# Performance work log

Measured on AMD Instinct MI355X. Metric: run time of the kernel, lower is better.

The kernel has to match this reference:

```python
import jax, jax.numpy as jnp
import numpy as np

B, SQ, SK, D = 8, 512, 512, 32


def _spd_cov(key, b, s, d):
    # random SPD covariance: A A^T + I
    a = 0.1 * jax.random.normal(key, (b, s, d, d), dtype=jnp.float32)
    return jnp.einsum('bsde,bsfe->bsdf', a, a) + jnp.eye(d, dtype=jnp.float32)


def setup_inputs() -> dict:
    key = jax.random.key(0)
    ks = jax.random.split(key, 6)
    return {
        'q_mean': jax.random.normal(ks[0], (B, SQ, D), dtype=jnp.float32),
        'q_cov': _spd_cov(ks[1], B, SQ, D),
        'k_mean': jax.random.normal(ks[2], (B, SK, D), dtype=jnp.float32),
        'k_cov': _spd_cov(ks[3], B, SK, D),
        'v_mean': jax.random.normal(ks[4], (B, SK, D), dtype=jnp.float32),
        'v_cov': _spd_cov(ks[5], B, SK, D),
    }


def reference(q_mean, q_cov, k_mean, k_cov, v_mean, v_cov):
    # Pairwise symmetric Gaussian JSD attention.
    # JSD = 0.5*(KL(p_q||p_k)+KL(p_k||p_q)); the log-det terms cancel:
    # JSD = 0.25*( tr(Sk^-1 Sq) + tr(Sq^-1 Sk) - 2D
    #              + dm^T (Sk^-1 + Sq^-1) dm ),  dm = mu_q - mu_k
    d = q_mean.shape[-1]
    q_inv = jnp.linalg.inv(q_cov)            # [B,Sq,D,D]
    k_inv = jnp.linalg.inv(k_cov)            # [B,Sk,D,D]
    tr_kq = jnp.einsum('bkde,bqed->bqk', k_inv, q_cov)
    tr_qk = jnp.einsum('bqde,bked->bqk', q_inv, k_cov)
    dm = q_mean[:, :, None, :] - k_mean[:, None, :, :]   # [B,Sq,Sk,D]
    quad = (jnp.einsum('bqkd,bkde,bqke->bqk', dm, k_inv, dm)
            + jnp.einsum('bqkd,bqde,bqke->bqk', dm, q_inv, dm))
    js = 0.25 * (tr_kq + tr_qk - 2.0 * d + quad)         # [B,Sq,Sk]
    score = jax.nn.softmax(js, axis=-1)
    out_mean = jnp.einsum('bqk,bkd->bqd', score, v_mean)
    out_cov = jnp.einsum('bqk,bkde->bqde', score, v_cov)
    return out_mean, out_cov
```

## Files before the change

### kernel.cpp

```cpp
#include <hip/hip_runtime.h>

#define NBATCH 8
#define SQL 512
#define SKL 512
#define DD 32
#define KF 1152
#define UT 528
#define NOUT 1056
#define NVT 1088

typedef short short8 __attribute__((ext_vector_type(8)));
typedef float f32x4 __attribute__((ext_vector_type(4)));
typedef unsigned short ushort_t;

__device__ __forceinline__ ushort_t f2bf(float f) {
    unsigned int u = __float_as_uint(f);
    return (ushort_t)((u + 0x7fffu + ((u >> 16) & 1u)) >> 16);
}
__device__ __forceinline__ float bf2f(ushort_t h) {
    return __uint_as_float(((unsigned int)h) << 16);
}
__device__ __forceinline__ void wsplit(ushort_t* __restrict__ h, ushort_t* __restrict__ l,
                                       size_t idx, float v) {
    ushort_t hb = f2bf(v);
    h[idx] = hb;
    l[idx] = f2bf(v - bf2f(hb));
}
__device__ __forceinline__ float rdlane(float x, int l) {
    return __int_as_float(__builtin_amdgcn_readlane(__float_as_int(x), l));
}
__device__ __forceinline__ void gl_lds16(const ushort_t* g, ushort_t* l) {
    __builtin_amdgcn_global_load_lds(
        (const __attribute__((address_space(1))) void*)g,
        (__attribute__((address_space(3))) void*)l, 16, 0, 0);
}

__global__ __launch_bounds__(256, 8) void feat_kernel(
    const float* __restrict__ qm, const float* __restrict__ qc,
    const float* __restrict__ km, const float* __restrict__ kc,
    ushort_t* __restrict__ fqh, ushort_t* __restrict__ fql,
    ushort_t* __restrict__ fkh, ushort_t* __restrict__ fkl)
{
    const int wid = threadIdx.x >> 6;
    const int lane = threadIdx.x & 63;
    const int gsite = blockIdx.x * 4 + wid;
    const int qside = gsite < NBATCH * SQL;
    const int site = qside ? gsite : gsite - NBATCH * SQL;

    const float* mean = qside ? qm : km;
    const float* cov  = qside ? qc : kc;
    ushort_t* fh = qside ? fqh : fkh;
    ushort_t* fl = qside ? fql : fkl;

    const float* covp = cov + (size_t)site * (DD * DD);
    const float* mup  = mean + (size_t)site * DD;
    const size_t fo = (size_t)site * KF;

    __shared__ float inv_s4[4][DD][DD + 1];
    __shared__ float mu_s4[4][DD];
    __shared__ float iv_s4[4][DD];
    float (*inv_s)[DD + 1] = inv_s4[wid];
    float* mu_s = mu_s4[wid];
    float* iv_s = iv_s4[wid];

    if (lane < DD) mu_s[lane] = mup[lane];

    float a[DD];
    if (lane < DD) {
        #pragma unroll
        for (int r = 0; r < DD; ++r) a[r] = covp[r * DD + lane];
    } else {
        const int c = lane - DD;
        #pragma unroll
        for (int r = 0; r < DD; ++r) a[r] = (r == c) ? 1.0f : 0.0f;
    }

    #pragma unroll
    for (int p = 0; p < DD; ++p) {
        float piv = rdlane(a[p], p);
        float rinv = 1.0f / piv;
        float t = a[p] * rinv;
        #pragma unroll
        for (int r = 0; r < DD; ++r) {
            if (r != p) {
                float fr = rdlane(a[r], p);
                a[r] = fmaf(-fr, t, a[r]);
            }
        }
        a[p] = t;
    }

    if (lane >= DD) {
        const int c = lane - DD;
        #pragma unroll
        for (int r = 0; r < DD; ++r) inv_s[r][c] = a[r];
    }
    __syncthreads();

    if (lane < DD) {
        float s = 0.f;
        #pragma unroll
        for (int e = 0; e < DD; ++e) s += inv_s[lane][e] * mu_s[e];
        iv_s[lane] = s;
    }
    __syncthreads();

    float bias = 0.f;
    #pragma unroll
    for (int d2 = 0; d2 < DD; ++d2) bias += mu_s[d2] * iv_s[d2];

    for (int idx = lane; idx < UT; idx += 64) {
        int d = (int)((65.0f - sqrtf(4225.0f - 8.0f * (float)idx)) * 0.5f);
        if (d > 0 && (d * (65 - d)) / 2 > idx) --d;
        if (((d + 1) * (64 - d)) / 2 <= idx) ++d;
        int off = (d * (65 - d)) / 2;
        int e = d + (idx - off);
        float Mv = covp[d * DD + e] + mu_s[d] * mu_s[e];
        float Iv = 0.5f * (inv_s[d][e] + inv_s[e][d]);
        float w = (d == e) ? 0.25f : 0.5f;
        if (qside) { wsplit(fh, fl, fo + idx, w * Mv); wsplit(fh, fl, fo + UT + idx, w * Iv); }
        else       { wsplit(fh, fl, fo + idx, Iv);     wsplit(fh, fl, fo + UT + idx, Mv); }
    }
    if (lane < DD) {
        float ivv = iv_s[lane], muv = mu_s[lane];
        if (qside) { wsplit(fh, fl, fo + 2*UT + lane, -0.5f * ivv); wsplit(fh, fl, fo + 2*UT + DD + lane, 0.25f * muv); }
        else       { wsplit(fh, fl, fo + 2*UT + lane, muv);         wsplit(fh, fl, fo + 2*UT + DD + lane, -2.f * ivv); }
    }
    if (lane == 32) wsplit(fh, fl, fo + 2*UT + 2*DD, qside ? 0.25f : bias);
    for (int i = 2*UT + 2*DD + 1 + lane; i < KF; i += 64) { fh[fo + i] = 0; fl[fo + i] = 0; }
}

template<int KSTRIDE, int KITERS, int MODE>
__global__ __launch_bounds__(256) void gemm_split(
    const ushort_t* __restrict__ Ah_g, const ushort_t* __restrict__ Al_g,
    const ushort_t* __restrict__ Bh_g, const ushort_t* __restrict__ Bl_g,
    float* __restrict__ C0, float* __restrict__ C1)
{
    constexpr bool ASPLIT = (MODE == 0);
    const int b = blockIdx.z, mt = blockIdx.y, nt = blockIdx.x;
    const int tid = threadIdx.x, lane = tid & 63, wid = tid >> 6;
    const int wm = wid & 1, wn = wid >> 1;
    const int BROWS = MODE ? NVT : SKL;

    const ushort_t* Ah = Ah_g + ((size_t)b * SQL + mt * 128) * KSTRIDE;
    const ushort_t* Al = Al_g + ((size_t)b * SQL + mt * 128) * KSTRIDE;
    const ushort_t* Bh = Bh_g + ((size_t)b * BROWS + nt * 64) * KSTRIDE;
    const ushort_t* Bl = Bl_g + ((size_t)b * BROWS + nt * 64) * KSTRIDE;

    __shared__ __align__(16) ushort_t AsH[128 * 32];
    __shared__ __align__(16) ushort_t AsL[ASPLIT ? 128 * 32 : 8];
    __shared__ __align__(16) ushort_t BsH[64 * 32];
    __shared__ __align__(16) ushort_t BsL[64 * 32];

    const int r4 = lane >> 2, kp = (lane & 3) * 8;
    const int arow0 = wid * 16 + r4,        aoff0 = wid * 512 + lane * 8;
    const int arow1 = (wid + 4) * 16 + r4,  aoff1 = (wid + 4) * 512 + lane * 8;

    const int fm = lane & 15;
    const int q8 = (lane >> 4) * 8;

    f32x4 acc[4][2];
    #pragma unroll
    for (int i = 0; i < 4; ++i)
        #pragma unroll
        for (int j = 0; j < 2; ++j)
            acc[i][j] = (f32x4){0.f, 0.f, 0.f, 0.f};

    for (int it = 0; it < KITERS; ++it) {
        const int k0 = it * 32;
        __syncthreads();
        gl_lds16(Ah + (size_t)arow0 * KSTRIDE + k0 + kp, &AsH[aoff0]);
        gl_lds16(Ah + (size_t)arow1 * KSTRIDE + k0 + kp, &AsH[aoff1]);
        if (ASPLIT) {
            gl_lds16(Al + (size_t)arow0 * KSTRIDE + k0 + kp, &AsL[aoff0]);
            gl_lds16(Al + (size_t)arow1 * KSTRIDE + k0 + kp, &AsL[aoff1]);
        }
        gl_lds16(Bh + (size_t)arow0 * KSTRIDE + k0 + kp, &BsH[aoff0]);
        gl_lds16(Bl + (size_t)arow0 * KSTRIDE + k0 + kp, &BsL[aoff0]);
        __syncthreads();

        short8 ah[4], al[4], bh[2], bl[2];
        #pragma unroll
        for (int i = 0; i < 4; ++i) {
            const int r = wm * 64 + i * 16 + fm;
            ah[i] = *(const short8*)&AsH[r * 32 + q8];
            if (ASPLIT) al[i] = *(const short8*)&AsL[r * 32 + q8];
        }
        #pragma unroll
        for (int j = 0; j < 2; ++j) {
            const int r = wn * 32 + j * 16 + fm;
            bh[j] = *(const short8*)&BsH[r * 32 + q8];
            bl[j] = *(const short8*)&BsL[r * 32 + q8];
        }
        #pragma unroll
        for (int i = 0; i < 4; ++i)
            #pragma unroll
            for (int j = 0; j < 2; ++j) {
                acc[i][j] = __builtin_amdgcn_mfma_f32_16x16x32_bf16(ah[i], bh[j], acc[i][j], 0, 0, 0);
                acc[i][j] = __builtin_amdgcn_mfma_f32_16x16x32_bf16(ah[i], bl[j], acc[i][j], 0, 0, 0);
                if (ASPLIT)
                    acc[i][j] = __builtin_amdgcn_mfma_f32_16x16x32_bf16(al[i], bh[j], acc[i][j], 0, 0, 0);
            }
    }

    const int crow0 = (lane >> 4) * 4;
    const int ccol = lane & 15;
    #pragma unroll
    for (int i = 0; i < 4; ++i) {
        const int m = mt * 128 + wm * 64 + i * 16 + crow0;
        #pragma unroll
        for (int j = 0; j < 2; ++j) {
            const int n = nt * 64 + wn * 32 + j * 16 + ccol;
            #pragma unroll
            for (int r = 0; r < 4; ++r) {
                const float v = acc[i][j][r];
                const size_t rowb = (size_t)b * SQL + (m + r);
                if (MODE == 0) {
                    C0[rowb * SKL + n] = v;
                } else {
                    if (n < DD)        C0[rowb * DD + n] = v;
                    else if (n < NOUT) C1[rowb * (DD * DD) + (n - DD)] = v;
                }
            }
        }
    }
}

__global__ __launch_bounds__(256) void softmax_rows(
    const float* __restrict__ js, ushort_t* __restrict__ ph)
{
    const float* p = js + (size_t)blockIdx.x * SKL;
    const int tid = threadIdx.x;
    float2 v = *(const float2*)(p + 2 * tid);
    float m = fmaxf(v.x, v.y);
    #pragma unroll
    for (int o = 32; o > 0; o >>= 1) m = fmaxf(m, __shfl_xor(m, o));
    __shared__ float redm[4], reds[4];
    const int wid = tid >> 6, ln = tid & 63;
    if (ln == 0) redm[wid] = m;
    __syncthreads();
    m = fmaxf(fmaxf(redm[0], redm[1]), fmaxf(redm[2], redm[3]));
    float e0 = __expf(v.x - m), e1 = __expf(v.y - m);
    float s = e0 + e1;
    #pragma unroll
    for (int o = 32; o > 0; o >>= 1) s += __shfl_xor(s, o);
    if (ln == 0) reds[wid] = s;
    __syncthreads();
    s = reds[0] + reds[1] + reds[2] + reds[3];
    float rs = 1.0f / s;
    size_t o = (size_t)blockIdx.x * SKL + 2 * tid;
    ph[o]     = f2bf(e0 * rs);
    ph[o + 1] = f2bf(e1 * rs);
}

__global__ __launch_bounds__(256) void vsplit_kernel(
    const float* __restrict__ vmean, const float* __restrict__ vcov,
    ushort_t* __restrict__ vth, ushort_t* __restrict__ vtl)
{
    __shared__ float t[32][33];
    const int n0 = blockIdx.x * 32, k0 = blockIdx.y * 32, b = blockIdx.z;
    const int tx = threadIdx.x, ty = threadIdx.y;
    for (int r = ty; r < 32; r += 8) {
        const int k = k0 + r, n = n0 + tx;
        float v;
        if (n0 == 0)          v = vmean[((size_t)b * SKL + k) * DD + n];
        else if (n0 >= NOUT)  v = 0.f;
        else                  v = vcov[((size_t)b * SKL + k) * (DD * DD) + (n - DD)];
        t[tx][r] = v;
    }
    __syncthreads();
    for (int r = ty; r < 32; r += 8) {
        const int n = n0 + r, k = k0 + tx;
        const float v = t[r][tx];
        wsplit(vth, vtl, ((size_t)b * NVT + n) * SKL + k, v);
    }
}

extern "C" void kernel_launch(void* const* d_in, const int* in_sizes, int n_in,
                              void* d_out, int out_size, void* d_ws, size_t ws_size,
                              hipStream_t stream)
{
    const float* q_mean = (const float*)d_in[0];
    const float* q_cov  = (const float*)d_in[1];
    const float* k_mean = (const float*)d_in[2];
    const float* k_cov  = (const float*)d_in[3];
    const float* v_mean = (const float*)d_in[4];
    const float* v_cov  = (const float*)d_in[5];

    float* out_mean = (float*)d_out;
    float* out_cov  = out_mean + (size_t)NBATCH * SQL * DD;

    char* w = (char*)d_ws;
    const size_t FQN = (size_t)NBATCH * SQL * KF;
    ushort_t* fq_h = (ushort_t*)w;
    ushort_t* fq_l = fq_h + FQN;
    ushort_t* fk_h = fq_l + FQN;
    ushort_t* fk_l = fk_h + FQN;
    float*    js   = (float*)(fk_l + FQN);
    ushort_t* vt_h = fq_h;
    ushort_t* vt_l = fq_l;
    ushort_t* p_h  = fk_h;

    feat_kernel<<<dim3(2 * NBATCH * SQL / 4), 256, 0, stream>>>(
        q_mean, q_cov, k_mean, k_cov, fq_h, fq_l, fk_h, fk_l);
    gemm_split<KF, KF / 32, 0><<<dim3(SKL / 64, SQL / 128, NBATCH), 256, 0, stream>>>(
        fq_h, fq_l, fk_h, fk_l, js, nullptr);
    vsplit_kernel<<<dim3(NVT / 32, SKL / 32, NBATCH), dim3(32, 8), 0, stream>>>(
        v_mean, v_cov, vt_h, vt_l);
    softmax_rows<<<NBATCH * SQL, 256, 0, stream>>>(js, p_h);
    gemm_split<SKL, SKL / 32, 1><<<dim3(NVT / 64, SQL / 128, NBATCH), 256, 0, stream>>>(
        p_h, nullptr, vt_h, vt_l, out_mean, out_cov);
}
```

Measured before the change: 225.1 us.

## Split-K score GEMM, drop bf16 low part for V GEMM, fuse softmax and V transpose

The score GEMM now splits K into two halves across more blocks and accumulates into a zeroed buffer with atomicAdd, which raises parallelism at the cost of a memset and atomics. The output GEMM drops the low-order bf16 correction for V and uses a single MFMA per tile, removing one MFMA and one LDS stream but lowering output precision. Softmax and the V transpose are merged into one launch to save a launch. The feature kernel stores the inverse in a packed upper-triangular layout and converts values in pairs to bf16.

```diff
diff --git a/kernel.cpp b/kernel.cpp
--- a/kernel.cpp
+++ b/kernel.cpp
@@ -1,4 +1,5 @@
 #include <hip/hip_runtime.h>
+#include <hip/hip_bf16.h>
 
 #define NBATCH 8
 #define SQL 512
@@ -8,6 +9,9 @@
 #define UT 528
 #define NOUT 1056
 #define NVT 1088
+#define NSITE (NBATCH * SQL)
+#define FEAT_BLOCKS (2 * NSITE / 4)
+#define VS_BLOCKS (34 * 16 * NBATCH)
 
 typedef short short8 __attribute__((ext_vector_type(8)));
 typedef float f32x4 __attribute__((ext_vector_type(4)));
@@ -19,12 +23,6 @@
 }
 __device__ __forceinline__ float bf2f(ushort_t h) {
     return __uint_as_float(((unsigned int)h) << 16);
-}
-__device__ __forceinline__ void wsplit(ushort_t* __restrict__ h, ushort_t* __restrict__ l,
-                                       size_t idx, float v) {
-    ushort_t hb = f2bf(v);
-    h[idx] = hb;
-    l[idx] = f2bf(v - bf2f(hb));
 }
 __device__ __forceinline__ float rdlane(float x, int l) {
     return __int_as_float(__builtin_amdgcn_readlane(__float_as_int(x), l));
@@ -33,6 +31,15 @@
     __builtin_amdgcn_global_load_lds(
         (const __attribute__((address_space(1))) void*)g,
         (__attribute__((address_space(3))) void*)l, 16, 0, 0);
+}
+__device__ __forceinline__ void pk_split(float v0, float v1, ushort_t& h0, ushort_t& h1,
+                                         ushort_t& l0, ushort_t& l1) {
+    __hip_bfloat162 H = __float22bfloat162_rn(make_float2(v0, v1));
+    ushort2 hu = *(ushort2*)&H;
+    h0 = hu.x; h1 = hu.y;
+    __hip_bfloat162 L = __float22bfloat162_rn(make_float2(v0 - bf2f(hu.x), v1 - bf2f(hu.y)));
+    ushort2 lu = *(ushort2*)&L;
+    l0 = lu.x; l1 = lu.y;
 }
 
 __global__ __launch_bounds__(256, 8) void feat_kernel(
@@ -41,11 +48,12 @@
     ushort_t* __restrict__ fqh, ushort_t* __restrict__ fql,
     ushort_t* __restrict__ fkh, ushort_t* __restrict__ fkl)
 {
+    __shared__ float smem[4 * 624];
     const int wid = threadIdx.x >> 6;
     const int lane = threadIdx.x & 63;
     const int gsite = blockIdx.x * 4 + wid;
-    const int qside = gsite < NBATCH * SQL;
-    const int site = qside ? gsite : gsite - NBATCH * SQL;
+    const int qside = gsite < NSITE;
+    const int site = qside ? gsite : gsite - NSITE;
 
     const float* mean = qside ? qm : km;
     const float* cov  = qside ? qc : kc;
@@ -56,12 +64,9 @@
     const float* mup  = mean + (size_t)site * DD;
     const size_t fo = (size_t)site * KF;
 
-    __shared__ float inv_s4[4][DD][DD + 1];
-    __shared__ float mu_s4[4][DD];
-    __shared__ float iv_s4[4][DD];
-    float (*inv_s)[DD + 1] = inv_s4[wid];
-    float* mu_s = mu_s4[wid];
-    float* iv_s = iv_s4[wid];
+    float* inv_p = smem + wid * 624;
+    float* mu_s  = inv_p + 560;
+    float* iv_s  = mu_s + 32;
 
     if (lane < DD) mu_s[lane] = mup[lane];
 
@@ -93,15 +98,22 @@
     if (lane >= DD) {
         const int c = lane - DD;
         #pragma unroll
-        for (int r = 0; r < DD; ++r) inv_s[r][c] = a[r];
+        for (int r = 0; r < DD; ++r)
+            if (r <= c) inv_p[((r * (65 - r)) >> 1) + (c - r)] = a[r];
     }
     __syncthreads();
 
-    if (lane < DD) {
+    {
+        const int j = lane & 31;
+        const int basej = (j * (65 - j)) >> 1;
         float s = 0.f;
         #pragma unroll
-        for (int e = 0; e < DD; ++e) s += inv_s[lane][e] * mu_s[e];
-        iv_s[lane] = s;
+        for (int e = 0; e < DD; ++e) {
+            const int be = (e * (65 - e)) >> 1;
+            const int addr = (e < j) ? (be + (j - e)) : (basej + (e - j));
+            s += inv_p[addr] * mu_s[e];
+        }
+        if (lane < DD) iv_s[lane] = s;
     }
     __syncthreads();
 
@@ -116,28 +128,47 @@
         int off = (d * (65 - d)) / 2;
         int e = d + (idx - off);
         float Mv = covp[d * DD + e] + mu_s[d] * mu_s[e];
-        float Iv = 0.5f * (inv_s[d][e] + inv_s[e][d]);
+        float Iv = inv_p[idx];
         float w = (d == e) ? 0.25f : 0.5f;
-        if (qside) { wsplit(fh, fl, fo + idx, w * Mv); wsplit(fh, fl, fo + UT + idx, w * Iv); }
-        else       { wsplit(fh, fl, fo + idx, Iv);     wsplit(fh, fl, fo + UT + idx, Mv); }
+        float v0, v1;
+        if (qside) { v0 = w * Mv; v1 = w * Iv; }
+        else       { v0 = Iv;     v1 = Mv; }
+        ushort_t h0, h1, l0, l1;
+        pk_split(v0, v1, h0, h1, l0, l1);
+        fh[fo + idx] = h0; fh[fo + UT + idx] = h1;
+        fl[fo + idx] = l0; fl[fo + UT + idx] = l1;
     }
     if (lane < DD) {
         float ivv = iv_s[lane], muv = mu_s[lane];
-        if (qside) { wsplit(fh, fl, fo + 2*UT + lane, -0.5f * ivv); wsplit(fh, fl, fo + 2*UT + DD + lane, 0.25f * muv); }
-        else       { wsplit(fh, fl, fo + 2*UT + lane, muv);         wsplit(fh, fl, fo + 2*UT + DD + lane, -2.f * ivv); }
-    }
-    if (lane == 32) wsplit(fh, fl, fo + 2*UT + 2*DD, qside ? 0.25f : bias);
+        float v0, v1;
+        if (qside) { v0 = -0.5f * ivv; v1 = 0.25f * muv; }
+        else       { v0 = muv;         v1 = -2.f * ivv; }
+        ushort_t h0, h1, l0, l1;
+        pk_split(v0, v1, h0, h1, l0, l1);
+        fh[fo + 2*UT + lane] = h0; fh[fo + 2*UT + DD + lane] = h1;
+        fl[fo + 2*UT + lane] = l0; fl[fo + 2*UT + DD + lane] = l1;
+    }
+    if (lane == 32) {
+        float v = qside ? 0.25f : bias;
+        ushort_t hb = f2bf(v);
+        fh[fo + 2*UT + 2*DD] = hb;
+        fl[fo + 2*UT + 2*DD] = f2bf(v - bf2f(hb));
+    }
     for (int i = 2*UT + 2*DD + 1 + lane; i < KF; i += 64) { fh[fo + i] = 0; fl[fo + i] = 0; }
 }
 
-template<int KSTRIDE, int KITERS, int MODE>
+template<int MODE>
 __global__ __launch_bounds__(256) void gemm_split(
     const ushort_t* __restrict__ Ah_g, const ushort_t* __restrict__ Al_g,
     const ushort_t* __restrict__ Bh_g, const ushort_t* __restrict__ Bl_g,
     float* __restrict__ C0, float* __restrict__ C1)
 {
-    constexpr bool ASPLIT = (MODE == 0);
-    const int b = blockIdx.z, mt = blockIdx.y, nt = blockIdx.x;
+    constexpr bool SPLIT = (MODE == 0);
+    constexpr int KSTRIDE = SPLIT ? KF : SKL;
+    constexpr int KITERS = SPLIT ? (KF / 2 / 32) : (SKL / 32);
+    const int b = blockIdx.z, nt = blockIdx.x;
+    const int mt = SPLIT ? (blockIdx.y & 3) : blockIdx.y;
+    const int kbase = SPLIT ? ((blockIdx.y >> 2) * (KF / 2)) : 0;
     const int tid = threadIdx.x, lane = tid & 63, wid = tid >> 6;
     const int wm = wid & 1, wn = wid >> 1;
     const int BROWS = MODE ? NVT : SKL;
@@ -148,9 +179,9 @@
     const ushort_t* Bl = Bl_g + ((size_t)b * BROWS + nt * 64) * KSTRIDE;
 
     __shared__ __align__(16) ushort_t AsH[128 * 32];
-    __shared__ __align__(16) ushort_t AsL[ASPLIT ? 128 * 32 : 8];
+    __shared__ __align__(16) ushort_t AsL[SPLIT ? 128 * 32 : 8];
     __shared__ __align__(16) ushort_t BsH[64 * 32];
-    __shared__ __align__(16) ushort_t BsL[64 * 32];
+    __shared__ __align__(16) ushort_t BsL[SPLIT ? 64 * 32 : 8];
 
     const int r4 = lane >> 2, kp = (lane & 3) * 8;
     const int arow0 = wid * 16 + r4,        aoff0 = wid * 512 + lane * 8;
@@ -167,16 +198,16 @@
             acc[i][j] = (f32x4){0.f, 0.f, 0.f, 0.f};
 
     for (int it = 0; it < KITERS; ++it) {
-        const int k0 = it * 32;
+        const int k0 = kbase + it * 32;
         __syncthreads();
         gl_lds16(Ah + (size_t)arow0 * KSTRIDE + k0 + kp, &AsH[aoff0]);
         gl_lds16(Ah + (size_t)arow1 * KSTRIDE + k0 + kp, &AsH[aoff1]);
-        if (ASPLIT) {
+        gl_lds16(Bh + (size_t)arow0 * KSTRIDE + k0 + kp, &BsH[aoff0]);
+        if (SPLIT) {
             gl_lds16(Al + (size_t)arow0 * KSTRIDE + k0 + kp, &AsL[aoff0]);
             gl_lds16(Al + (size_t)arow1 * KSTRIDE + k0 + kp, &AsL[aoff1]);
-        }
-        gl_lds16(Bh + (size_t)arow0 * KSTRIDE + k0 + kp, &BsH[aoff0]);
-        gl_lds16(Bl + (size_t)arow0 * KSTRIDE + k0 + kp, &BsL[aoff0]);
+            gl_lds16(Bl + (size_t)arow0 * KSTRIDE + k0 + kp, &BsL[aoff0]);
+        }
         __syncthreads();
 
         short8 ah[4], al[4], bh[2], bl[2];
@@ -184,22 +215,23 @@
         for (int i = 0; i < 4; ++i) {
             const int r = wm * 64 + i * 16 + fm;
             ah[i] = *(const short8*)&AsH[r * 32 + q8];
-            if (ASPLIT) al[i] = *(const short8*)&AsL[r * 32 + q8];
+            if (SPLIT) al[i] = *(const short8*)&AsL[r * 32 + q8];
         }
         #pragma unroll
         for (int j = 0; j < 2; ++j) {
             const int r = wn * 32 + j * 16 + fm;
             bh[j] = *(const short8*)&BsH[r * 32 + q8];
-            bl[j] = *(const short8*)&BsL[r * 32 + q8];
+            if (SPLIT) bl[j] = *(const short8*)&BsL[r * 32 + q8];
         }
         #pragma unroll
         for (int i = 0; i < 4; ++i)
             #pragma unroll
             for (int j = 0; j < 2; ++j) {
                 acc[i][j] = __builtin_amdgcn_mfma_f32_16x16x32_bf16(ah[i], bh[j], acc[i][j], 0, 0, 0);
-                acc[i][j] = __builtin_amdgcn_mfma_f32_16x16x32_bf16(ah[i], bl[j], acc[i][j], 0, 0, 0);
-                if (ASPLIT)
+                if (SPLIT) {
+                    acc[i][j] = __builtin_amdgcn_mfma_f32_16x16x32_bf16(ah[i], bl[j], acc[i][j], 0, 0, 0);
                     acc[i][j] = __builtin_amdgcn_mfma_f32_16x16x32_bf16(al[i], bh[j], acc[i][j], 0, 0, 0);
+                }
             }
     }
 
@@ -216,7 +248,7 @@
                 const float v = acc[i][j][r];
                 const size_t rowb = (size_t)b * SQL + (m + r);
                 if (MODE == 0) {
-                    C0[rowb * SKL + n] = v;
+                    atomicAdd(&C0[rowb * SKL + n], v);
                 } else {
                     if (n < DD)        C0[rowb * DD + n] = v;
                     else if (n < NOUT) C1[rowb * (DD * DD) + (n - DD)] = v;
@@ -226,53 +258,53 @@
     }
 }
 
-__global__ __launch_bounds__(256) void softmax_rows(
-    const float* __restrict__ js, ushort_t* __restrict__ ph)
+__global__ __launch_bounds__(256) void phase2_kernel(
+    const float* __restrict__ js, ushort_t* __restrict__ ph,
+    const float* __restrict__ vmean, const float* __restrict__ vcov,
+    ushort_t* __restrict__ vth)
 {
-    const float* p = js + (size_t)blockIdx.x * SKL;
+    __shared__ float sm[32 * 33];
     const int tid = threadIdx.x;
-    float2 v = *(const float2*)(p + 2 * tid);
-    float m = fmaxf(v.x, v.y);
-    #pragma unroll
-    for (int o = 32; o > 0; o >>= 1) m = fmaxf(m, __shfl_xor(m, o));
-    __shared__ float redm[4], reds[4];
-    const int wid = tid >> 6, ln = tid & 63;
-    if (ln == 0) redm[wid] = m;
-    __syncthreads();
-    m = fmaxf(fmaxf(redm[0], redm[1]), fmaxf(redm[2], redm[3]));
-    float e0 = __expf(v.x - m), e1 = __expf(v.y - m);
-    float s = e0 + e1;
-    #pragma unroll
-    for (int o = 32; o > 0; o >>= 1) s += __shfl_xor(s, o);
-    if (ln == 0) reds[wid] = s;
-    __syncthreads();
-    s = reds[0] + reds[1] + reds[2] + reds[3];
-    float rs = 1.0f / s;
-    size_t o = (size_t)blockIdx.x * SKL + 2 * tid;
-    ph[o]     = f2bf(e0 * rs);
-    ph[o + 1] = f2bf(e1 * rs);
-}
-
-__global__ __launch_bounds__(256) void vsplit_kernel(
-    const float* __restrict__ vmean, const float* __restrict__ vcov,
-    ushort_t* __restrict__ vth, ushort_t* __restrict__ vtl)
-{
-    __shared__ float t[32][33];
-    const int n0 = blockIdx.x * 32, k0 = blockIdx.y * 32, b = blockIdx.z;
-    const int tx = threadIdx.x, ty = threadIdx.y;
-    for (int r = ty; r < 32; r += 8) {
-        const int k = k0 + r, n = n0 + tx;
-        float v;
-        if (n0 == 0)          v = vmean[((size_t)b * SKL + k) * DD + n];
-        else if (n0 >= NOUT)  v = 0.f;
-        else                  v = vcov[((size_t)b * SKL + k) * (DD * DD) + (n - DD)];
-        t[tx][r] = v;
-    }
-    __syncthreads();
-    for (int r = ty; r < 32; r += 8) {
-        const int n = n0 + r, k = k0 + tx;
-        const float v = t[r][tx];
-        wsplit(vth, vtl, ((size_t)b * NVT + n) * SKL + k, v);
+    if (blockIdx.x < (unsigned)(NBATCH * SQL)) {
+        const float* p = js + (size_t)blockIdx.x * SKL;
+        float2 v = *(const float2*)(p + 2 * tid);
+        float m = fmaxf(v.x, v.y);
+        #pragma unroll
+        for (int o = 32; o > 0; o >>= 1) m = fmaxf(m, __shfl_xor(m, o));
+        const int wid = tid >> 6, ln = tid & 63;
+        if (ln == 0) sm[wid] = m;
+        __syncthreads();
+        m = fmaxf(fmaxf(sm[0], sm[1]), fmaxf(sm[2], sm[3]));
+        float e0 = __expf(v.x - m), e1 = __expf(v.y - m);
+        float s = e0 + e1;
+        #pragma unroll
+        for (int o = 32; o > 0; o >>= 1) s += __shfl_xor(s, o);
+        if (ln == 0) sm[4 + wid] = s;
+        __syncthreads();
+        s = sm[4] + sm[5] + sm[6] + sm[7];
+        float rs = 1.0f / s;
+        size_t o = (size_t)blockIdx.x * SKL + 2 * tid;
+        ph[o]     = f2bf(e0 * rs);
+        ph[o + 1] = f2bf(e1 * rs);
+    } else {
+        const int vb = blockIdx.x - NBATCH * SQL;
+        const int b = vb / (34 * 16), rem = vb % (34 * 16);
+        const int kt = rem / 34, nt = rem % 34;
+        const int n0 = nt * 32, k0 = kt * 32;
+        const int tx = tid & 31, ty = tid >> 5;
+        for (int r = ty; r < 32; r += 8) {
+            const int k = k0 + r, n = n0 + tx;
+            float v;
+            if (n0 == 0)          v = vmean[((size_t)b * SKL + k) * DD + n];
+            else if (n0 >= NOUT)  v = 0.f;
+            else                  v = vcov[((size_t)b * SKL + k) * (DD * DD) + (n - DD)];
+            sm[tx * 33 + r] = v;
+        }
+        __syncthreads();
+        for (int r = ty; r < 32; r += 8) {
+            const int n = n0 + r, k = k0 + tx;
+            vth[((size_t)b * NVT + n) * SKL + k] = f2bf(sm[r * 33 + tx]);
+        }
     }
 }
 
@@ -298,16 +330,15 @@
     ushort_t* fk_l = fk_h + FQN;
     float*    js   = (float*)(fk_l + FQN);
     ushort_t* vt_h = fq_h;
-    ushort_t* vt_l = fq_l;
     ushort_t* p_h  = fk_h;
 
-    feat_kernel<<<dim3(2 * NBATCH * SQL / 4), 256, 0, stream>>>(
+    feat_kernel<<<FEAT_BLOCKS, 256, 0, stream>>>(
         q_mean, q_cov, k_mean, k_cov, fq_h, fq_l, fk_h, fk_l);
-    gemm_split<KF, KF / 32, 0><<<dim3(SKL / 64, SQL / 128, NBATCH), 256, 0, stream>>>(
+    hipMemsetAsync(js, 0, (size_t)NBATCH * SQL * SKL * sizeof(float), stream);
+    gemm_split<0><<<dim3(SKL / 64, 8, NBATCH), 256, 0, stream>>>(
         fq_h, fq_l, fk_h, fk_l, js, nullptr);
-    vsplit_kernel<<<dim3(NVT / 32, SKL / 32, NBATCH), dim3(32, 8), 0, stream>>>(
-        v_mean, v_cov, vt_h, vt_l);
-    softmax_rows<<<NBATCH * SQL, 256, 0, stream>>>(js, p_h);
-    gemm_split<SKL, SKL / 32, 1><<<dim3(NVT / 64, SQL / 128, NBATCH), 256, 0, stream>>>(
-        p_h, nullptr, vt_h, vt_l, out_mean, out_cov);
-}
+    phase2_kernel<<<NBATCH * SQL + VS_BLOCKS, 256, 0, stream>>>(
+        js, p_h, v_mean, v_cov, vt_h);
+    gemm_split<1><<<dim3(NVT / 64, SQL / 128, NBATCH), 256, 0, stream>>>(
+        p_h, nullptr, vt_h, nullptr, out_mean, out_cov);
+}
```

Result: faster. 218.0 us (-3.2%).
